# Optimization experiments

Hardware: AMD Instinct MI355X
Metric: run time of the kernel (lower is better)

The kernel has to match this reference:

```python
import jax, jax.numpy as jnp
import numpy as np

B, D, L, NH = 8, 1024, 1024, 8
DK = D // NH  # = Dv = 128
NEG = -1e30


def setup_inputs() -> dict:
    key = jax.random.key(0)
    kx, km, kq, kk, kv, ko = jax.random.split(key, 6)
    x = jax.random.normal(kx, (B, D, L), dtype=jnp.float32)
    # binary mask over sequence positions (float, as in the torch code)
    mask = (jax.random.uniform(km, (B, L)) > 0.1).astype(jnp.float32)
    # xavier-ish scale for per-head projections, kaiming-ish for Wo
    s_qkv = np.sqrt(2.0 / (D + DK)).astype(np.float32)
    Wq = jax.random.normal(kq, (NH, D, DK), dtype=jnp.float32) * s_qkv
    Wk = jax.random.normal(kk, (NH, D, DK), dtype=jnp.float32) * s_qkv
    Wv = jax.random.normal(kv, (NH, D, DK), dtype=jnp.float32) * s_qkv
    Wo = jax.random.normal(ko, (D, DK * NH), dtype=jnp.float32) * np.sqrt(2.0 / D).astype(np.float32)
    return {"x": x, "mask": mask, "Wq": Wq, "Wk": Wk, "Wv": Wv, "Wo": Wo}


def reference(x, mask, Wq, Wk, Wv, Wo):
    # x: [B, D, L] -> [B, L, D]
    xt = jnp.swapaxes(x, 1, 2)
    scale = 1.0 / np.sqrt(DK).astype(np.float32)
    # batched per-head projections (equivalent to the per-head loop)
    q = jnp.einsum("bld,hdk->bhlk", xt, Wq)  # [B,H,L,Dk]
    k = jnp.einsum("bld,hdk->bhlk", xt, Wk)
    v = jnp.einsum("bld,hdk->bhlk", xt, Wv)
    # scores[b,h,q_pos,k_pos]
    scores = jnp.einsum("bhqd,bhkd->bhqk", q, k) * scale
    # mask.unsqueeze(2) in torch -> additive mask along the QUERY axis
    scores = scores + (1.0 - mask)[:, None, :, None] * NEG
    # faithful quirk: softmax over dim=1 of [B,Lq,Lk] == query axis (axis=2 here)
    attn = jax.nn.softmax(scores, axis=2)
    heads = jnp.einsum("bhqk,bhkd->bhqd", attn, v)  # [B,H,L,Dv]
    head = jnp.swapaxes(heads, 1, 2).reshape(B, L, NH * DK)  # concat heads
    out = head @ Wo  # [B, L, D]
    return jnp.swapaxes(out, 1, 2)  # [B, D, L]
```

## Files before the change

### kernel.cpp

```cpp
#include <hip/hip_runtime.h>

typedef short bf16x8 __attribute__((ext_vector_type(8)));
typedef float f32x4 __attribute__((ext_vector_type(4)));

#define MASK_NEG (-1e30f)

__device__ __forceinline__ unsigned short f2bf(float f) {
  union { float f; unsigned u; } v; v.f = f;
  unsigned r = v.u + 0x7fffu + ((v.u >> 16) & 1u);
  return (unsigned short)(r >> 16);
}

__device__ __forceinline__ float bf2f(unsigned short u) {
  union { unsigned u; float f; } v; v.u = ((unsigned)u) << 16;
  return v.f;
}

__device__ __forceinline__ void gl_lds16(const void* g, void* l) {
  __builtin_amdgcn_global_load_lds(
      (__attribute__((address_space(1))) void*)(void*)g,
      (__attribute__((address_space(3))) void*)l, 16, 0, 0);
}

__global__ __launch_bounds__(256) void transpose_f32_bf16(
    const float* __restrict__ src, unsigned short* __restrict__ dst,
    int R, int C, long sstride, long dstride) {
  __shared__ float tile[64][65];
  const int z = blockIdx.z;
  const float* s = src + (size_t)z * sstride;
  unsigned short* d = dst + (size_t)z * dstride;
  const int x0 = blockIdx.x * 64;
  const int y0 = blockIdx.y * 64;
  const int t = threadIdx.x;
  {
    const int r = t >> 4, c4 = (t & 15) * 4;
    for (int it = 0; it < 4; ++it) {
      const int rr = r + it * 16;
      const float4 v = *(const float4*)(s + (size_t)(y0 + rr) * C + x0 + c4);
      tile[rr][c4 + 0] = v.x; tile[rr][c4 + 1] = v.y;
      tile[rr][c4 + 2] = v.z; tile[rr][c4 + 3] = v.w;
    }
  }
  __syncthreads();
  {
    const int cc = t >> 4, r4 = (t & 15) * 4;
    for (int it = 0; it < 4; ++it) {
      const int c = cc + it * 16;
      ushort4 o;
      o.x = f2bf(tile[r4 + 0][c]); o.y = f2bf(tile[r4 + 1][c]);
      o.z = f2bf(tile[r4 + 2][c]); o.w = f2bf(tile[r4 + 3][c]);
      *(ushort4*)(d + (size_t)(x0 + c) * R + y0 + r4) = o;
    }
  }
}

template<bool F32OUT>
__global__ __launch_bounds__(256) void gemm_tn(
    const unsigned short* __restrict__ A, const unsigned short* __restrict__ B,
    void* __restrict__ Cv,
    int K, int ldA, int ldB, int ldC, float scale,
    long sAl, long sAb, long sAh,
    long sBl, long sBb, long sBh,
    long sCl, long sCb, long sCh,
    int zbase, int zdiv)
{
  __shared__ unsigned short As[4096];
  __shared__ unsigned short Bs[4096];
  const int z = blockIdx.z;
  const int g = zbase + z;
  const int gb = g / zdiv, gh = g % zdiv;
  const unsigned short* Ab = A + (size_t)z * sAl + (size_t)gb * sAb + (size_t)gh * sAh;
  const unsigned short* Bb = B + (size_t)z * sBl + (size_t)gb * sBb + (size_t)gh * sBh;
  const int m0 = blockIdx.y * 128, n0 = blockIdx.x * 128;
  const int t = threadIdx.x;
  const int lane = t & 63;
  const int wave = t >> 6;
  const int wm = wave >> 1, wn = wave & 1;

  const int sr = t >> 2;
  const int ss = t & 3;
  const int sq = ss ^ (sr & 3) ^ ((sr >> 2) & 3);

  const unsigned short* ap0 = Ab + (size_t)(m0 + sr) * ldA + sq * 8;
  const unsigned short* ap1 = Ab + (size_t)(m0 + sr + 64) * ldA + sq * 8;
  const unsigned short* bp0 = Bb + (size_t)(n0 + sr) * ldB + sq * 8;
  const unsigned short* bp1 = Bb + (size_t)(n0 + sr + 64) * ldB + sq * 8;

  char* asd0 = (char*)As + t * 16;
  char* asd1 = (char*)As + 4096 + t * 16;
  char* bsd0 = (char*)Bs + t * 16;
  char* bsd1 = (char*)Bs + 4096 + t * 16;

  const int tq = lane & 15, qd = lane >> 4;
  const int slot = qd ^ (tq & 3) ^ ((tq >> 2) & 3);

  f32x4 acc[4][4];
  #pragma unroll
  for (int i = 0; i < 4; ++i)
    #pragma unroll
    for (int j = 0; j < 4; ++j)
      acc[i][j] = f32x4{0.f, 0.f, 0.f, 0.f};

  const int kIters = K >> 5;
  for (int kt = 0; kt < kIters; ++kt) {
    __syncthreads();
    gl_lds16(ap0, asd0); gl_lds16(ap1, asd1);
    gl_lds16(bp0, bsd0); gl_lds16(bp1, bsd1);
    ap0 += 32; ap1 += 32; bp0 += 32; bp1 += 32;
    __builtin_amdgcn_s_waitcnt(0x0f70);
    __syncthreads();

    bf16x8 af[4], bfr[4];
    #pragma unroll
    for (int i = 0; i < 4; ++i)
      af[i] = *(const bf16x8*)(As + ((wm * 64 + i * 16 + tq) * 32 + slot * 8));
    #pragma unroll
    for (int j = 0; j < 4; ++j)
      bfr[j] = *(const bf16x8*)(Bs + ((wn * 64 + j * 16 + tq) * 32 + slot * 8));
    #pragma unroll
    for (int i = 0; i < 4; ++i)
      #pragma unroll
      for (int j = 0; j < 4; ++j)
        acc[i][j] = __builtin_amdgcn_mfma_f32_16x16x32_bf16(af[i], bfr[j], acc[i][j], 0, 0, 0);
  }

  const size_t cOff = (size_t)z * sCl + (size_t)gb * sCb + (size_t)gh * sCh;
  #pragma unroll
  for (int i = 0; i < 4; ++i) {
    const int row = m0 + wm * 64 + i * 16 + qd * 4;
    #pragma unroll
    for (int j = 0; j < 4; ++j) {
      const int col = n0 + wn * 64 + j * 16 + tq;
      if constexpr (F32OUT) {
        float* C = (float*)Cv + cOff;
        #pragma unroll
        for (int rr = 0; rr < 4; ++rr)
          C[(size_t)(row + rr) * ldC + col] = acc[i][j][rr] * scale;
      } else {
        unsigned short* C = (unsigned short*)Cv + cOff;
        #pragma unroll
        for (int rr = 0; rr < 4; ++rr)
          C[(size_t)(row + rr) * ldC + col] = f2bf(acc[i][j][rr] * scale);
      }
    }
  }
}

__global__ __launch_bounds__(256) void gemm_scores_fused(
    const unsigned short* __restrict__ QKV,
    unsigned short* __restrict__ E, float* __restrict__ colsum,
    const float* __restrict__ mask, int zbase)
{
  __shared__ unsigned short As[4096];
  __shared__ unsigned short Bs[4096];
  const int z = blockIdx.z;
  const int g = zbase + z;
  const int b = g >> 3, h = g & 7;
  const unsigned short* Ab = QKV + (size_t)b * 3145728 + (size_t)h * 131072;
  const unsigned short* Bb = Ab + 1048576;
  const int m0 = blockIdx.y * 128, n0 = blockIdx.x * 128;
  const int t = threadIdx.x;
  const int lane = t & 63;
  const int wave = t >> 6;
  const int wm = wave >> 1, wn = wave & 1;

  const int sr = t >> 2, ss = t & 3;
  const int sq = ss ^ (sr & 3) ^ ((sr >> 2) & 3);

  const unsigned short* ap0 = Ab + (size_t)(m0 + sr) * 128 + sq * 8;
  const unsigned short* ap1 = Ab + (size_t)(m0 + sr + 64) * 128 + sq * 8;
  const unsigned short* bp0 = Bb + (size_t)(n0 + sr) * 128 + sq * 8;
  const unsigned short* bp1 = Bb + (size_t)(n0 + sr + 64) * 128 + sq * 8;

  char* asd0 = (char*)As + t * 16;
  char* asd1 = (char*)As + 4096 + t * 16;
  char* bsd0 = (char*)Bs + t * 16;
  char* bsd1 = (char*)Bs + 4096 + t * 16;

  const int tq = lane & 15, qd = lane >> 4;
  const int slot = qd ^ (tq & 3) ^ ((tq >> 2) & 3);

  f32x4 acc[4][4];
  #pragma unroll
  for (int i = 0; i < 4; ++i)
    #pragma unroll
    for (int j = 0; j < 4; ++j)
      acc[i][j] = f32x4{0.f, 0.f, 0.f, 0.f};

  #pragma unroll
  for (int kt = 0; kt < 4; ++kt) {
    __syncthreads();
    gl_lds16(ap0, asd0); gl_lds16(ap1, asd1);
    gl_lds16(bp0, bsd0); gl_lds16(bp1, bsd1);
    ap0 += 32; ap1 += 32; bp0 += 32; bp1 += 32;
    __builtin_amdgcn_s_waitcnt(0x0f70);
    __syncthreads();

    bf16x8 af[4], bfr[4];
    #pragma unroll
    for (int i = 0; i < 4; ++i)
      af[i] = *(const bf16x8*)(As + ((wm * 64 + i * 16 + tq) * 32 + slot * 8));
    #pragma unroll
    for (int j = 0; j < 4; ++j)
      bfr[j] = *(const bf16x8*)(Bs + ((wn * 64 + j * 16 + tq) * 32 + slot * 8));
    #pragma unroll
    for (int i = 0; i < 4; ++i)
      #pragma unroll
      for (int j = 0; j < 4; ++j)
        acc[i][j] = __builtin_amdgcn_mfma_f32_16x16x32_bf16(af[i], bfr[j], acc[i][j], 0, 0, 0);
  }

  unsigned short* Ep = E + (size_t)z * 1048576;
  float* cs = colsum + (size_t)g * 1024;
  const float scl = 0.08838834764831845f;
  const float* mrow = mask + (size_t)b * 1024;

  float cp[4] = {0.f, 0.f, 0.f, 0.f};
  #pragma unroll
  for (int i = 0; i < 4; ++i) {
    const int row0 = m0 + wm * 64 + i * 16 + qd * 4;
    const float4 m4 = *(const float4*)(mrow + row0);
    const float aq[4] = {(1.f - m4.x) * MASK_NEG - 20.f, (1.f - m4.y) * MASK_NEG - 20.f,
                         (1.f - m4.z) * MASK_NEG - 20.f, (1.f - m4.w) * MASK_NEG - 20.f};
    #pragma unroll
    for (int rr = 0; rr < 4; ++rr) {
      unsigned short* erow = Ep + (size_t)(row0 + rr) * 1024 + n0 + wn * 64 + tq;
      #pragma unroll
      for (int j = 0; j < 4; ++j) {
        const float e = __expf(acc[i][j][rr] * scl + aq[rr]);
        cp[j] += e;
        erow[j * 16] = f2bf(e);
      }
    }
  }
  #pragma unroll
  for (int j = 0; j < 4; ++j) {
    float v = cp[j];
    v += __shfl_xor(v, 16, 64);
    v += __shfl_xor(v, 32, 64);
    if (qd == 0)
      atomicAdd(&cs[n0 + wn * 64 + j * 16 + tq], v);
  }
}

__global__ __launch_bounds__(256) void tvscale(
    const unsigned short* __restrict__ QKV, unsigned short* __restrict__ Vp,
    const float* __restrict__ colsum, int zbase)
{
  __shared__ unsigned short tile[64][72];
  const int z = blockIdx.z;
  const int g = zbase + z;
  const int b = g >> 3, h = g & 7;
  const unsigned short* S = QKV + (size_t)b * 3145728 + (size_t)(16 + h) * 131072;
  unsigned short* D = Vp + (size_t)g * 131072;
  const float* cs = colsum + (size_t)g * 1024;
  const int l0 = blockIdx.x * 64;
  const int d0 = blockIdx.y * 64;
  const int t = threadIdx.x;
  {
    const int r = t >> 4, c4 = (t & 15) * 4;
    for (int it = 0; it < 4; ++it) {
      const int rr = r + it * 16;
      const ushort4 v = *(const ushort4*)(S + (size_t)(l0 + rr) * 128 + d0 + c4);
      *(ushort4*)&tile[rr][c4] = v;
    }
  }
  __syncthreads();
  {
    const int cc = t >> 4, r4 = (t & 15) * 4;
    const float4 c4v = *(const float4*)(cs + l0 + r4);
    for (int it = 0; it < 4; ++it) {
      const int c = cc + it * 16;
      ushort4 o;
      o.x = f2bf(bf2f(tile[r4 + 0][c]) / c4v.x);
      o.y = f2bf(bf2f(tile[r4 + 1][c]) / c4v.y);
      o.z = f2bf(bf2f(tile[r4 + 2][c]) / c4v.z);
      o.w = f2bf(bf2f(tile[r4 + 3][c]) / c4v.w);
      *(ushort4*)(D + (size_t)(d0 + c) * 1024 + l0 + r4) = o;
    }
  }
}

extern "C" void kernel_launch(void* const* d_in, const int* in_sizes, int n_in,
                              void* d_out, int out_size, void* d_ws, size_t ws_size,
                              hipStream_t stream) {
  const float* x    = (const float*)d_in[0];
  const float* mask = (const float*)d_in[1];
  const float* Wq   = (const float*)d_in[2];
  const float* Wk   = (const float*)d_in[3];
  const float* Wv   = (const float*)d_in[4];
  const float* Wo   = (const float*)d_in[5];
  float* out = (float*)d_out;

  char* p = (char*)d_ws;
  unsigned short* xt    = (unsigned short*)p; p += 16777216;
  unsigned short* WqkvT = (unsigned short*)p; p += 6291456;
  unsigned short* Wot   = (unsigned short*)p; p += 2097152;
  unsigned short* QKV   = (unsigned short*)p; p += 50331648;
  unsigned short* Vp    = (unsigned short*)p; p += 16777216;
  unsigned short* Hp    = (unsigned short*)p; p += 16777216;
  float* colsum = (float*)p; p += 262144;
  const size_t fixedBytes = (size_t)(p - (char*)d_ws);

  long nbh = 1;
  if (ws_size > fixedBytes) {
    nbh = (long)((ws_size - fixedBytes) / 2097152);
    if (nbh < 1) nbh = 1;
    if (nbh > 64) nbh = 64;
  }
  unsigned short* Ep = (unsigned short*)p;

  hipMemsetAsync(colsum, 0, 262144, stream);

  transpose_f32_bf16<<<dim3(16, 16, 8), 256, 0, stream>>>(x,  xt,  1024, 1024, 1048576L, 1048576L);
  transpose_f32_bf16<<<dim3(2, 16, 8),  256, 0, stream>>>(Wq, WqkvT,           1024, 128, 131072L, 131072L);
  transpose_f32_bf16<<<dim3(2, 16, 8),  256, 0, stream>>>(Wk, WqkvT + 1048576, 1024, 128, 131072L, 131072L);
  transpose_f32_bf16<<<dim3(2, 16, 8),  256, 0, stream>>>(Wv, WqkvT + 2097152, 1024, 128, 131072L, 131072L);
  transpose_f32_bf16<<<dim3(16, 16, 1), 256, 0, stream>>>(Wo, Wot, 1024, 1024, 1048576L, 1048576L);

  gemm_tn<false><<<dim3(1, 8, 192), 256, 0, stream>>>(
      xt, WqkvT, (void*)QKV, 1024, 1024, 1024, 128, 1.f,
      0L, 1048576L, 0L,  0L, 0L, 131072L,  0L, 3145728L, 131072L, 0, 24);

  for (int s0 = 0; s0 < 64; s0 += (int)nbh) {
    const int cnt = (int)(((64 - s0) < nbh) ? (64 - s0) : nbh);
    gemm_scores_fused<<<dim3(8, 8, cnt), 256, 0, stream>>>(QKV, Ep, colsum, mask, s0);
    tvscale<<<dim3(16, 2, cnt), 256, 0, stream>>>(QKV, Vp, colsum, s0);
    gemm_tn<false><<<dim3(1, 8, cnt), 256, 0, stream>>>(
        Ep, Vp, (void*)Hp, 1024, 1024, 1024, 1024, 1.f,
        1048576L, 0L, 0L,  0L, 1048576L, 131072L,  0L, 1048576L, 128L, s0, 8);
  }
  gemm_tn<true><<<dim3(8, 8, 8), 256, 0, stream>>>(
      Wot, Hp, (void*)out, 1024, 1024, 1024, 1024, 1.f,
      0L, 0L, 0L,  0L, 1048576L, 0L,  0L, 1048576L, 0L, 0, 1);
}
```

Measured before the change: 316.9 us.

## Double GEMM K-tile to 64 and merge transpose launches into two kernels

The shared gemm_tn kernel now stages a 64-wide K slice per iteration instead of 32, using an 8-way XOR swizzle. Each barrier pair is followed by two MFMA sub-steps, which halves the number of synchronizations and load phases per output tile. Separately, the five input-transpose launches are merged into two kernels that select their source by blockIdx.z, which cuts launch overhead. The larger tile doubles LDS use per block (32 KB), which may reduce occupancy.

```diff
diff --git a/kernel.cpp b/kernel.cpp
--- a/kernel.cpp
+++ b/kernel.cpp
@@ -22,16 +22,9 @@
       (__attribute__((address_space(3))) void*)l, 16, 0, 0);
 }
 
-__global__ __launch_bounds__(256) void transpose_f32_bf16(
-    const float* __restrict__ src, unsigned short* __restrict__ dst,
-    int R, int C, long sstride, long dstride) {
-  __shared__ float tile[64][65];
-  const int z = blockIdx.z;
-  const float* s = src + (size_t)z * sstride;
-  unsigned short* d = dst + (size_t)z * dstride;
-  const int x0 = blockIdx.x * 64;
-  const int y0 = blockIdx.y * 64;
-  const int t = threadIdx.x;
+__device__ __forceinline__ void transpose_tile(
+    const float* __restrict__ s, unsigned short* __restrict__ d,
+    int R, int C, int x0, int y0, int t, float tile[64][65]) {
   {
     const int r = t >> 4, c4 = (t & 15) * 4;
     for (int it = 0; it < 4; ++it) {
@@ -52,6 +45,30 @@
       *(ushort4*)(d + (size_t)(x0 + c) * R + y0 + r4) = o;
     }
   }
+}
+
+__global__ __launch_bounds__(256) void transpose_x_wo(
+    const float* __restrict__ x, const float* __restrict__ Wo,
+    unsigned short* __restrict__ xt, unsigned short* __restrict__ Wot) {
+  __shared__ float tile[64][65];
+  const int z = blockIdx.z;
+  const float* s = (z < 8) ? (x + (size_t)z * 1048576) : Wo;
+  unsigned short* d = (z < 8) ? (xt + (size_t)z * 1048576) : Wot;
+  transpose_tile(s, d, 1024, 1024, blockIdx.x * 64, blockIdx.y * 64,
+                 threadIdx.x, tile);
+}
+
+__global__ __launch_bounds__(256) void transpose_w24(
+    const float* __restrict__ Wq, const float* __restrict__ Wk,
+    const float* __restrict__ Wv, unsigned short* __restrict__ WqkvT) {
+  __shared__ float tile[64][65];
+  const int z = blockIdx.z;
+  const int sel = z >> 3, h = z & 7;
+  const float* base = (sel == 0) ? Wq : (sel == 1) ? Wk : Wv;
+  const float* s = base + (size_t)h * 131072;
+  unsigned short* d = WqkvT + (size_t)z * 131072;
+  transpose_tile(s, d, 1024, 128, blockIdx.x * 64, blockIdx.y * 64,
+                 threadIdx.x, tile);
 }
 
 template<bool F32OUT>
@@ -64,8 +81,8 @@
     long sCl, long sCb, long sCh,
     int zbase, int zdiv)
 {
-  __shared__ unsigned short As[4096];
-  __shared__ unsigned short Bs[4096];
+  __shared__ unsigned short As[128 * 64];
+  __shared__ unsigned short Bs[128 * 64];
   const int z = blockIdx.z;
   const int g = zbase + z;
   const int gb = g / zdiv, gh = g % zdiv;
@@ -77,22 +94,29 @@
   const int wave = t >> 6;
   const int wm = wave >> 1, wn = wave & 1;
 
-  const int sr = t >> 2;
-  const int ss = t & 3;
-  const int sq = ss ^ (sr & 3) ^ ((sr >> 2) & 3);
-
-  const unsigned short* ap0 = Ab + (size_t)(m0 + sr) * ldA + sq * 8;
-  const unsigned short* ap1 = Ab + (size_t)(m0 + sr + 64) * ldA + sq * 8;
-  const unsigned short* bp0 = Bb + (size_t)(n0 + sr) * ldB + sq * 8;
-  const unsigned short* bp1 = Bb + (size_t)(n0 + sr + 64) * ldB + sq * 8;
-
-  char* asd0 = (char*)As + t * 16;
-  char* asd1 = (char*)As + 4096 + t * 16;
-  char* bsd0 = (char*)Bs + t * 16;
-  char* bsd1 = (char*)Bs + 4096 + t * 16;
+  const int sr2 = t >> 3;
+  const int ss8 = t & 7;
+  const int sq8 = ss8 ^ (sr2 & 7);
+
+  const unsigned short* ap0 = Ab + (size_t)(m0 +  0 + sr2) * ldA + sq8 * 8;
+  const unsigned short* ap1 = Ab + (size_t)(m0 + 32 + sr2) * ldA + sq8 * 8;
+  const unsigned short* ap2 = Ab + (size_t)(m0 + 64 + sr2) * ldA + sq8 * 8;
+  const unsigned short* ap3 = Ab + (size_t)(m0 + 96 + sr2) * ldA + sq8 * 8;
+  const unsigned short* bp0 = Bb + (size_t)(n0 +  0 + sr2) * ldB + sq8 * 8;
+  const unsigned short* bp1 = Bb + (size_t)(n0 + 32 + sr2) * ldB + sq8 * 8;
+  const unsigned short* bp2 = Bb + (size_t)(n0 + 64 + sr2) * ldB + sq8 * 8;
+  const unsigned short* bp3 = Bb + (size_t)(n0 + 96 + sr2) * ldB + sq8 * 8;
+
+  char* asd0 = (char*)As +     0 + t * 16;
+  char* asd1 = (char*)As +  4096 + t * 16;
+  char* asd2 = (char*)As +  8192 + t * 16;
+  char* asd3 = (char*)As + 12288 + t * 16;
+  char* bsd0 = (char*)Bs +     0 + t * 16;
+  char* bsd1 = (char*)Bs +  4096 + t * 16;
+  char* bsd2 = (char*)Bs +  8192 + t * 16;
+  char* bsd3 = (char*)Bs + 12288 + t * 16;
 
   const int tq = lane & 15, qd = lane >> 4;
-  const int slot = qd ^ (tq & 3) ^ ((tq >> 2) & 3);
 
   f32x4 acc[4][4];
   #pragma unroll
@@ -101,27 +125,39 @@
     for (int j = 0; j < 4; ++j)
       acc[i][j] = f32x4{0.f, 0.f, 0.f, 0.f};
 
-  const int kIters = K >> 5;
+  const int kIters = K >> 6;
   for (int kt = 0; kt < kIters; ++kt) {
     __syncthreads();
     gl_lds16(ap0, asd0); gl_lds16(ap1, asd1);
+    gl_lds16(ap2, asd2); gl_lds16(ap3, asd3);
     gl_lds16(bp0, bsd0); gl_lds16(bp1, bsd1);
-    ap0 += 32; ap1 += 32; bp0 += 32; bp1 += 32;
+    gl_lds16(bp2, bsd2); gl_lds16(bp3, bsd3);
+    ap0 += 64; ap1 += 64; ap2 += 64; ap3 += 64;
+    bp0 += 64; bp1 += 64; bp2 += 64; bp3 += 64;
     __builtin_amdgcn_s_waitcnt(0x0f70);
     __syncthreads();
 
-    bf16x8 af[4], bfr[4];
-    #pragma unroll
-    for (int i = 0; i < 4; ++i)
-      af[i] = *(const bf16x8*)(As + ((wm * 64 + i * 16 + tq) * 32 + slot * 8));
-    #pragma unroll
-    for (int j = 0; j < 4; ++j)
-      bfr[j] = *(const bf16x8*)(Bs + ((wn * 64 + j * 16 + tq) * 32 + slot * 8));
-    #pragma unroll
-    for (int i = 0; i < 4; ++i)
-      #pragma unroll
-      for (int j = 0; j < 4; ++j)
-        acc[i][j] = __builtin_amdgcn_mfma_f32_16x16x32_bf16(af[i], bfr[j], acc[i][j], 0, 0, 0);
+    #pragma unroll
+    for (int kk = 0; kk < 2; ++kk) {
+      bf16x8 af[4], bfr[4];
+      #pragma unroll
+      for (int i = 0; i < 4; ++i) {
+        const int R = wm * 64 + i * 16 + tq;
+        const int slot = (kk * 4 + qd) ^ (R & 7);
+        af[i] = *(const bf16x8*)(As + R * 64 + slot * 8);
+      }
+      #pragma unroll
+      for (int j = 0; j < 4; ++j) {
+        const int R = wn * 64 + j * 16 + tq;
+        const int slot = (kk * 4 + qd) ^ (R & 7);
+        bfr[j] = *(const bf16x8*)(Bs + R * 64 + slot * 8);
+      }
+      #pragma unroll
+      for (int i = 0; i < 4; ++i)
+        #pragma unroll
+        for (int j = 0; j < 4; ++j)
+          acc[i][j] = __builtin_amdgcn_mfma_f32_16x16x32_bf16(af[i], bfr[j], acc[i][j], 0, 0, 0);
+    }
   }
 
   const size_t cOff = (size_t)z * sCl + (size_t)gb * sCb + (size_t)gh * sCh;
@@ -312,11 +348,8 @@
 
   hipMemsetAsync(colsum, 0, 262144, stream);
 
-  transpose_f32_bf16<<<dim3(16, 16, 8), 256, 0, stream>>>(x,  xt,  1024, 1024, 1048576L, 1048576L);
-  transpose_f32_bf16<<<dim3(2, 16, 8),  256, 0, stream>>>(Wq, WqkvT,           1024, 128, 131072L, 131072L);
-  transpose_f32_bf16<<<dim3(2, 16, 8),  256, 0, stream>>>(Wk, WqkvT + 1048576, 1024, 128, 131072L, 131072L);
-  transpose_f32_bf16<<<dim3(2, 16, 8),  256, 0, stream>>>(Wv, WqkvT + 2097152, 1024, 128, 131072L, 131072L);
-  transpose_f32_bf16<<<dim3(16, 16, 1), 256, 0, stream>>>(Wo, Wot, 1024, 1024, 1048576L, 1048576L);
+  transpose_x_wo<<<dim3(16, 16, 9), 256, 0, stream>>>(x, Wo, xt, Wot);
+  transpose_w24<<<dim3(2, 16, 24), 256, 0, stream>>>(Wq, Wk, Wv, WqkvT);
 
   gemm_tn<false><<<dim3(1, 8, 192), 256, 0, stream>>>(
       xt, WqkvT, (void*)QKV, 1024, 1024, 1024, 128, 1.f,
```

Result: faster. 298.0 us (-6.0%).
